# Kernel optimization log

Measured on AMD Instinct MI355X. Metric: run time of the kernel, lower is better.

Reference implementation:

```python
import jax, jax.numpy as jnp
import numpy as np

B, T, I, H, D, C, OUT = 32, 128, 64, 256, 32, 64, 32
DECAY = 0.99

def _lin(k, fi, fo):
    lim = 1.0 / np.sqrt(fi)
    kw, kb = jax.random.split(k)
    W = jax.random.uniform(kw, (fi, fo), minval=-lim, maxval=lim, dtype=jnp.float32)
    b = jax.random.uniform(kb, (fo,), minval=-lim, maxval=lim, dtype=jnp.float32)
    return W, b

def setup_inputs():
    key = jax.random.key(0)
    ks = jax.random.split(key, 12)
    x = jax.random.normal(ks[0], (B, T, I), dtype=jnp.float32)
    lengths = jax.random.randint(ks[1], (B,), 1, T + 1)
    W_dg1, b_dg1 = _lin(ks[2], I + H, D)
    W_dg2, b_dg2 = _lin(ks[3], D, D)
    W_e1, b_e1 = _lin(ks[4], 2 * I, H)
    W_e2, b_e2 = _lin(ks[5], H, H)
    W_ih, b_ih = _lin(ks[6], H, 3 * H)
    W_hh, b_hh = _lin(ks[7], H, 3 * H)
    W_f1, b_f1 = _lin(ks[8], H, H)
    W_f2, b_f2 = _lin(ks[9], H, C)
    return dict(x=x, lengths=lengths, out_lengths=OUT,
                W_dg1=W_dg1, b_dg1=b_dg1, W_dg2=W_dg2, b_dg2=b_dg2,
                W_e1=W_e1, b_e1=b_e1, W_e2=W_e2, b_e2=b_e2,
                W_ih=W_ih, b_ih=b_ih, W_hh=W_hh, b_hh=b_hh,
                W_f1=W_f1, b_f1=b_f1, W_f2=W_f2, b_f2=b_f2)

def _forward(x, lengths, out_lengths, W_dg1, b_dg1, W_dg2, b_dg2, W_e1, b_e1, W_e2, b_e2,
             W_ih, b_ih, W_hh, b_hh, W_f1, b_f1, W_f2, b_f2):
    Bs, Ts, Is = x.shape
    Ds = W_dg2.shape[1]
    Hs = W_e2.shape[1]
    decay = DECAY ** jnp.arange(1, Ds + 1, dtype=x.dtype)  # [D]
    d_idx = jnp.arange(Ds)
    gkey = jax.random.key(42)
    g_enc = jax.random.gumbel(jax.random.fold_in(gkey, 0), (Ts, Bs, Ds), x.dtype)
    g_dec = jax.random.gumbel(jax.random.fold_in(gkey, 1), (out_lengths, Bs, Ds), x.dtype)
    masks = (jnp.arange(Ts)[None, :] < lengths[:, None]).astype(x.dtype)  # [B,T]

    def gumbel_softmax_hard(logits, g):
        # F.gumbel_softmax(..., tau=1.0, hard=True) straight-through estimator
        y_soft = jax.nn.softmax(logits + g, axis=-1)
        y_hard = jax.nn.one_hot(jnp.argmax(y_soft, axis=-1), Ds, dtype=logits.dtype)
        return y_hard + y_soft - jax.lax.stop_gradient(y_soft)

    def gru_cell(xin, h):
        # torch.nn.GRUCell gate order: r, z, n
        gi = xin @ W_ih + b_ih
        gh = h @ W_hh + b_hh
        i_r, i_z, i_n = jnp.split(gi, 3, axis=-1)
        h_r, h_z, h_n = jnp.split(gh, 3, axis=-1)
        r = jax.nn.sigmoid(i_r + h_r)
        z = jax.nn.sigmoid(i_z + h_z)
        n = jnp.tanh(i_n + r * h_n)
        return (1.0 - z) * n + z * h

    def step_core(buf, h, x_t, g_t, mem_t):
        cell_in = jnp.concatenate([x_t, h], axis=-1)
        logits = jax.nn.elu(cell_in @ W_dg1 + b_dg1) @ W_dg2 + b_dg2
        gate = gumbel_softmax_hard(logits, g_t)  # [B,D]
        # shift buffer along dim 1 (new[:, :-1] = old[:, 1:], last slot zeroed)
        new_buf = jnp.concatenate([buf[:, 1:], jnp.zeros_like(buf[:, :1])], axis=1)
        upd = x_t[:, None, :] * decay[None, :, None] * gate[:, :, None]  # [B,D,I]
        new_buf = new_buf.at[:, d_idx, d_idx].set(upd)  # diagonal scatter-assign
        rnn_in = jnp.concatenate([x_t, mem_t], axis=-1)
        rnn_in = jax.nn.elu(rnn_in @ W_e1 + b_e1) @ W_e2 + b_e2
        return new_buf, gru_cell(rnn_in, h)

    buf0 = jnp.zeros((Bs, Ds + 1, Ds, Is), x.dtype)
    h0 = jnp.zeros((Bs, Hs), x.dtype)

    def enc_step(carry, inp):
        buf, h = carry
        x_t, m_t, g_t = inp
        mem_t = buf[:, 0].sum(axis=1)  # [B,I]
        buf, nh = step_core(buf, h, x_t, g_t, mem_t)
        h = m_t[:, None] * nh + (1.0 - m_t[:, None]) * h
        return (buf, h), None

    (buf, h), _ = jax.lax.scan(enc_step, (buf0, h0),
                               (jnp.swapaxes(x, 0, 1), masks.T, g_enc))

    x_zero = jnp.zeros((Bs, Is), x.dtype)

    def dec_step(carry, g_t):
        buf, h = carry
        # get_current_memory(slide=True): roll -1 along dim1 with last slot zeroed
        buf = jnp.concatenate([buf[:, 1:], jnp.zeros_like(buf[:, :1])], axis=1)
        mem_t = buf[:, 0].sum(axis=1)
        buf, nh = step_core(buf, h, x_zero, g_t, mem_t)
        out = jax.nn.relu(nh @ W_f1 + b_f1) @ W_f2 + b_f2
        return (buf, nh), out

    _, outs = jax.lax.scan(dec_step, (buf, h), g_dec)  # [OUT,B,C]
    return jnp.swapaxes(outs, 0, 1)  # [B,OUT,C]

def reference(x, lengths, out_lengths, W_dg1, b_dg1, W_dg2, b_dg2, W_e1, b_e1, W_e2, b_e2,
              W_ih, b_ih, W_hh, b_hh, W_f1, b_f1, W_f2, b_f2):
    return _forward(x, lengths, out_lengths, W_dg1, b_dg1, W_dg2, b_dg2, W_e1, b_e1,
                    W_e2, b_e2, W_ih, b_ih, W_hh, b_hh, W_f1, b_f1, W_f2, b_f2)
```

## Files before the change

### kernel.cpp

```cpp
#include <hip/hip_runtime.h>
#include <math.h>


#define kB 32
#define kT 128
#define kI 64
#define kH 256
#define kD 32
#define kC 64
#define kOut 32
#define kSteps (kT + kOut)
#define NB 89
#define NTHR 256
#define NT_ALL (NB * NTHR)

#define WS_FL    384
#define WS_H     1856
#define WS_SEL   (WS_H + 4*8192)
#define WS_MEM   (WS_SEL + 128)
#define WS_NZ    (WS_MEM + kB*kSteps*kI)
#define WS_LIN   WS_NZ
#define WS_O1    (WS_LIN + 4*8192)
#define WS_W2    (WS_O1 + 4*8192)
#define WS_B2    (WS_W2 + kH*3*kH)
#define WS_G     (WS_B2 + 3*kH)
#define WS_P     (WS_G + kT*kB*kD)
#define WS_ZERO_BYTES ((size_t)WS_NZ * sizeof(float))

__device__ __forceinline__ float cload(const float* p) {
  return __hip_atomic_load(p, __ATOMIC_RELAXED, __HIP_MEMORY_SCOPE_AGENT);
}
__device__ __forceinline__ void cstore(float* p, float v) {
  __hip_atomic_store(p, v, __ATOMIC_RELAXED, __HIP_MEMORY_SCOPE_AGENT);
}
__device__ __forceinline__ int cload_i(const int* p) {
  return __hip_atomic_load(p, __ATOMIC_RELAXED, __HIP_MEMORY_SCOPE_AGENT);
}
__device__ __forceinline__ void cstore_i(int* p, int v) {
  __hip_atomic_store(p, v, __ATOMIC_RELAXED, __HIP_MEMORY_SCOPE_AGENT);
}
__device__ __forceinline__ float4 cload4(const float* p) {
  float4 r;
  asm volatile("global_load_dwordx4 %0, %1, off sc0 sc1" : "=v"(r) : "v"(p));
  return r;
}
__device__ __forceinline__ void waitvm() {
  asm volatile("s_waitcnt vmcnt(0)" ::: "memory");
}

__device__ __forceinline__ void poll(const int* FL, int tid,
                                     int tH, int tDG, int tE, int tF1, int tF2) {
  int thr;
  if      (tid < 32) thr = tH;
  else if (tid == 32) thr = tDG;
  else if (tid < 65) thr = tE;
  else if (tid < 81) thr = tF1;
  else if (tid < 89) thr = tF2;
  else thr = 0;
  const int* p = FL + tid * 16;
  for (;;) {
    int ok = (thr <= 0) || (cload_i(p) >= thr);
    if (__syncthreads_count(ok) == NTHR) return;
    __builtin_amdgcn_s_sleep(2);
  }
}
__device__ __forceinline__ void setflag(int* FL, int tid, int idx, int val) {
  waitvm();
  __syncthreads();
  if (tid == 0) cstore_i(FL + idx * 16, val);
}

__device__ __forceinline__ void tf2x32(unsigned k0, unsigned k1,
                                       unsigned x0, unsigned x1,
                                       unsigned& o0, unsigned& o1) {
  unsigned ks2 = k0 ^ k1 ^ 0x1BD11BDAu;
  unsigned v0 = x0 + k0, v1 = x1 + k1;
#define TFR(r) { v0 += v1; v1 = (v1 << (r)) | (v1 >> (32-(r))); v1 ^= v0; }
  TFR(13) TFR(15) TFR(26) TFR(6)   v0 += k1;  v1 += ks2 + 1u;
  TFR(17) TFR(29) TFR(16) TFR(24)  v0 += ks2; v1 += k0  + 2u;
  TFR(13) TFR(15) TFR(26) TFR(6)   v0 += k0;  v1 += k1  + 3u;
  TFR(17) TFR(29) TFR(16) TFR(24)  v0 += k1;  v1 += ks2 + 4u;
  TFR(13) TFR(15) TFR(26) TFR(6)   v0 += ks2; v1 += k0  + 5u;
#undef TFR
  o0 = v0; o1 = v1;
}
__device__ __forceinline__ float bits_to_gumbel(unsigned bits) {
  float f = __uint_as_float((bits >> 9) | 0x3F800000u) - 1.0f;
  float u = f + 1.17549435e-38f;
  return -logf(-logf(u));
}

__device__ __forceinline__ void gridbar_full(unsigned* u, unsigned target) {
  __syncthreads();
  if (threadIdx.x == 0) {
    __threadfence();
    __hip_atomic_fetch_add(&u[320], 1u, __ATOMIC_ACQ_REL, __HIP_MEMORY_SCOPE_AGENT);
    while (__hip_atomic_load(&u[320], __ATOMIC_RELAXED, __HIP_MEMORY_SCOPE_AGENT) < target)
      __builtin_amdgcn_s_sleep(1);
    __threadfence();
  }
  __syncthreads();
}

__device__ __forceinline__ float elu1(float v) { return v > 0.f ? v : expm1f(v); }

__global__ __launch_bounds__(NTHR)
void delay_rnn(const float* __restrict__ x, const int* __restrict__ lengths,
               const float* __restrict__ W_dg1, const float* __restrict__ b_dg1,
               const float* __restrict__ W_dg2, const float* __restrict__ b_dg2,
               const float* __restrict__ W_e1,  const float* __restrict__ b_e1,
               const float* __restrict__ W_e2,  const float* __restrict__ b_e2,
               const float* __restrict__ W_ih,  const float* __restrict__ b_ih,
               const float* __restrict__ W_hh,  const float* __restrict__ b_hh,
               const float* __restrict__ W_f1,  const float* __restrict__ b_f1,
               const float* __restrict__ W_f2,  const float* __restrict__ b_f2,
               float* __restrict__ out, float* __restrict__ ws) {
  const int tid = threadIdx.x;
  const int bid = blockIdx.x;
  const int gid = bid * NTHR + tid;

  unsigned* baru = (unsigned*)ws;
  int*   FL    = (int*)(ws + WS_FL);
  float* hBuf  = ws + WS_H;
  int*   selG  = (int*)(ws + WS_SEL);
  float* mem   = ws + WS_MEM;
  float* linB  = ws + WS_LIN;
  float* o1B   = ws + WS_O1;
  float* W2g   = ws + WS_W2;
  float* B2g   = ws + WS_B2;
  float* g     = ws + WS_G;
  float* Pg    = ws + WS_P;

  __shared__ float S[35264];
  __shared__ float lgarr[1056];
  __shared__ float sb1[32], sb2[32], dec_sh[32];
  __shared__ int   sel[32], len_s[32];

  {
    unsigned k0, k1;
    tf2x32(0u, 42u, 0u, 0u, k0, k1);
    for (int i = gid; i < kT * kB * kD; i += NT_ALL) {
      unsigned a, b;
      tf2x32(k0, k1, 0u, (unsigned)i, a, b);
      g[i] = bits_to_gumbel(a ^ b);
    }
  }
  for (int idx = gid; idx < kH * 3 * kH; idx += NT_ALL) {
    int k = idx / (3 * kH), n = idx % (3 * kH);
    const float* wr = W_e2 + k * kH;
    float s0 = 0, s1 = 0, s2 = 0, s3 = 0;
    for (int m = 0; m < kH; m += 4) {
      float4 wv = *(const float4*)(wr + m);
      s0 += wv.x * W_ih[(m    ) * 3 * kH + n];
      s1 += wv.y * W_ih[(m + 1) * 3 * kH + n];
      s2 += wv.z * W_ih[(m + 2) * 3 * kH + n];
      s3 += wv.w * W_ih[(m + 3) * 3 * kH + n];
    }
    W2g[idx] = ((s0 + s1) + (s2 + s3));
  }
  for (int n = gid; n < 3 * kH; n += NT_ALL) {
    float s = b_ih[n];
    for (int m = 0; m < kH; ++m) s += b_e2[m] * W_ih[m * 3 * kH + n];
    B2g[n] = s;
  }
  for (int idx = gid; idx < kT * kB * kH; idx += NT_ALL) {
    int s = idx >> 13, r = idx & 8191, b = r >> 8, j = r & 255;
    const float* xr = x + (b * kT + s) * kI;
    float a0 = 0, a1 = 0, a2 = 0, a3 = 0;
    for (int k = 0; k < 64; k += 4) {
      float4 xv = *(const float4*)(xr + k);
      a0 += xv.x * W_e1[(64 + k) * 256 + j];
      a1 += xv.y * W_e1[(65 + k) * 256 + j];
      a2 += xv.z * W_e1[(66 + k) * 256 + j];
      a3 += xv.w * W_e1[(67 + k) * 256 + j];
    }
    Pg[idx] = ((a0 + a1) + (a2 + a3));
  }

  gridbar_full(baru, NB);

  if (bid < 32) {
    float* whh = S; float* w2 = S + 6240;
    const int jb = bid * 8;
    for (int i = tid; i < 6144; i += NTHR) {
      int gg = i >> 11, r = i & 2047, jj = r >> 8, k = r & 255;
      whh[(gg * 8 + jj) * 260 + k] = W_hh[k * 768 + gg * 256 + jb + jj];
      w2 [(gg * 8 + jj) * 260 + k] = W2g [k * 768 + gg * 256 + jb + jj];
    }
    if (tid < 24) { int gg = tid / 8, jj = tid % 8;
      sb1[tid] = b_hh[gg * 256 + jb + jj];
      sb2[tid] = B2g [gg * 256 + jb + jj];
    }
    if (tid < 32) len_s[tid] = lengths[tid];
    __syncthreads();

    float* sH = S + 12480; float* sLin = S + 20800;
    float* red = S + 29120;
    for (int s = 0; s < kSteps; ++s) {
      int tDG = (s >= 1) ? (s < kT ? s : kT) : 0;
      int tF1 = (s >= kT + 4) ? (s - 2) : 0;
      poll(FL, tid, s, tDG, s + 1, tF1, 0);

      const float* hR = hBuf + (s & 3) * 8192;
      const float* lR = linB + (s & 3) * 8192;
      const bool useC = (s >= 1 && s < kT);
      const float4* P4 = (const float4*)(Pg + (s - 1) * 8192);
      const int* selR = selG + ((s - 1) & 3) * 32;
      float4 th[8], tl[8], tp[8];
      int tsel[8];
      #pragma unroll
      for (int u8 = 0; u8 < 8; ++u8) {
        int i4 = (tid + u8 * 256) * 4;
        th[u8] = cload4(hR + i4);
        tl[u8] = cload4(lR + i4);
      }
      if (useC) {
        #pragma unroll
        for (int u8 = 0; u8 < 8; ++u8) {
          int idx = tid + u8 * 256; int b = idx >> 6, k4 = idx & 63;
          tp[u8] = P4[b * 64 + k4];
          tsel[u8] = cload_i(&selR[b]);
        }
      }
      waitvm();
      #pragma unroll
      for (int u8 = 0; u8 < 8; ++u8) {
        int idx = tid + u8 * 256; int b = idx >> 6, k4 = idx & 63;
        *(float4*)&sH[b * 260 + k4 * 4] = th[u8];
        float cx = 0.f, cy = 0.f, cz = 0.f, cw = 0.f;
        if (useC && tsel[u8] == 0) {
          cx = 0.99f * tp[u8].x; cy = 0.99f * tp[u8].y;
          cz = 0.99f * tp[u8].z; cw = 0.99f * tp[u8].w;
        }
        float4 v;
        v.x = elu1(tl[u8].x + cx);
        v.y = elu1(tl[u8].y + cy);
        v.z = elu1(tl[u8].z + cz);
        v.w = elu1(tl[u8].w + cw);
        *(float4*)&sLin[b * 260 + k4 * 4] = v;
      }
      __syncthreads();
      const float4* sH4 = (const float4*)sH;
      const float4* sL4 = (const float4*)sLin;
      const float4* wh4 = (const float4*)whh;
      const float4* w24 = (const float4*)w2;
      const int c  = tid & 7;
      const int b4 = (tid >> 3) & 7;
      const int kq = tid >> 6;
      float acc[24];
      #pragma unroll
      for (int a = 0; a < 24; ++a) acc[a] = 0.f;
      for (int kk = 0; kk < 16; ++kk) {
        int k4 = kq * 16 + kk;
        float4 wr[6];
        #pragma unroll
        for (int gg = 0; gg < 3; ++gg) {
          wr[gg]     = wh4[(gg * 8 + c) * 65 + k4];
          wr[3 + gg] = w24[(gg * 8 + c) * 65 + k4];
        }
        #pragma unroll
        for (int bi = 0; bi < 4; ++bi) {
          int b = bi * 8 + b4;
          float4 h4 = sH4[b * 65 + k4];
          float4 l4 = sL4[b * 65 + k4];
          #pragma unroll
          for (int gg = 0; gg < 3; ++gg) {
            float4 w = wr[gg];
            acc[bi * 6 + gg]     += h4.x * w.x + h4.y * w.y + h4.z * w.z + h4.w * w.w;
            w = wr[3 + gg];
            acc[bi * 6 + 3 + gg] += l4.x * w.x + l4.y * w.y + l4.z * w.z + l4.w * w.w;
          }
        }
      }
      #pragma unroll
      for (int bi = 0; bi < 4; ++bi)
        #pragma unroll
        for (int rr = 0; rr < 6; ++rr)
          red[kq * 1536 + rr * 256 + (bi * 8 + b4) * 8 + c] = acc[bi * 6 + rr];
      __syncthreads();
      {
        int b = tid >> 3, cc = tid & 7, jg = bid * 8 + cc;
        int lo = b * 8 + cc;
        float dots[6];
        #pragma unroll
        for (int rr = 0; rr < 6; ++rr)
          dots[rr] = (red[rr * 256 + lo] + red[1536 + rr * 256 + lo]) +
                     (red[3072 + rr * 256 + lo] + red[4608 + rr * 256 + lo]);
        float ghr = dots[0] + sb1[cc];
        float ghz = dots[1] + sb1[8 + cc];
        float ghn = dots[2] + sb1[16 + cc];
        float gir = dots[3] + sb2[cc];
        float giz = dots[4] + sb2[8 + cc];
        float gin = dots[5] + sb2[16 + cc];
        float r = 1.f / (1.f + expf(-(gir + ghr)));
        float z = 1.f / (1.f + expf(-(giz + ghz)));
        float n = tanhf(gin + r * ghn);
        float hold = sH[b * 260 + jg];
        float nh = (1.f - z) * n + z * hold;
        float hv = (s < kT) ? ((s < len_s[b]) ? nh : hold) : nh;
        cstore(&hBuf[((s + 1) & 3) * 8192 + b * 256 + jg], hv);
      }
      setflag(FL, tid, bid, s + 1);
    }
  }
  else if (bid < 64) {
    float* we1 = S;
    const int jb = (bid - 32) * 8;
    for (int i = tid; i < 1024; i += NTHR) {
      int jj = i >> 7, k = i & 127;
      we1[jj * 132 + k] = W_e1[k * 256 + jb + jj];
    }
    if (tid < 8) sb1[tid] = b_e1[jb + tid];
    __syncthreads();

    float* sx = S + 1056; float* sm = S + 3232;
    for (int e = 0; e < kSteps; ++e) {
      int tDG = e - 1 < 0 ? 0 : (e - 1 > kT ? kT : e - 1);
      poll(FL, tid, e - 2, tDG, 0, 0, 0);

      const bool encx = (e < kT);
      float4 tm[2];
      #pragma unroll
      for (int u2 = 0; u2 < 2; ++u2) {
        int idx = tid + u2 * 256; int b = idx >> 4, k4 = idx & 15;
        tm[u2] = cload4(mem + (b * kSteps + e) * kI + k4 * 4);
      }
      waitvm();
      #pragma unroll
      for (int u2 = 0; u2 < 2; ++u2) {
        int idx = tid + u2 * 256; int b = idx >> 4, k4 = idx & 15;
        *(float4*)&sm[b * 68 + k4 * 4] = tm[u2];
        if (encx)
          *(float4*)&sx[b * 68 + k4 * 4] =
              *(const float4*)(x + (b * kT + e) * kI + k4 * 4);
      }
      __syncthreads();
      const int b = tid >> 3, jj = tid & 7;
      const float4* sx4 = (const float4*)sx;
      const float4* sm4 = (const float4*)sm;
      const float4* w4p = (const float4*)we1;
      float a0 = 0, a1 = 0, a2 = 0, a3 = 0;
      if (encx) {
        for (int k4 = 0; k4 < 16; ++k4) {
          float4 xv = sx4[b * 17 + k4], w = w4p[jj * 33 + k4];
          a0 += xv.x * w.x; a1 += xv.y * w.y; a2 += xv.z * w.z; a3 += xv.w * w.w;
        }
      }
      for (int k4 = 0; k4 < 16; ++k4) {
        float4 mv = sm4[b * 17 + k4], w = w4p[jj * 33 + 16 + k4];
        a0 += mv.x * w.x; a1 += mv.y * w.y; a2 += mv.z * w.z; a3 += mv.w * w.w;
      }
      cstore(&linB[(e & 3) * 8192 + b * 256 + jb + jj],
             ((a0 + a1) + (a2 + a3)) + sb1[jj]);
      __syncthreads();
      setflag(FL, tid, 33 + (bid - 32), e + 1);
    }
  }
  else if (bid < 80) {
    float* wf1 = S;
    const int jb = (bid - 64) * 16;
    for (int i = tid; i < 4096; i += NTHR) {
      int jj = i >> 8, k = i & 255;
      wf1[jj * 260 + k] = W_f1[k * 256 + jb + jj];
    }
    if (tid < 16) sb1[tid] = b_f1[jb + tid];
    __syncthreads();

    float* sHf = S + 4160; float* red = S + 12480;
    for (int s = kT + 1; s <= kSteps; ++s) {
      int tF2 = (s >= kT + 5) ? (s - 2) : 0;
      poll(FL, tid, s, 0, 0, 0, tF2);

      const float* hR = hBuf + (s & 3) * 8192;
      float4 th[8];
      #pragma unroll
      for (int u8 = 0; u8 < 8; ++u8) th[u8] = cload4(hR + (tid + u8 * 256) * 4);
      waitvm();
      #pragma unroll
      for (int u8 = 0; u8 < 8; ++u8) {
        int idx = tid + u8 * 256; int b = idx >> 6, k4 = idx & 63;
        *(float4*)&sHf[b * 260 + k4 * 4] = th[u8];
      }
      __syncthreads();
      const float4* sH4 = (const float4*)sHf;
      const float4* w4p = (const float4*)wf1;
      const int cq = tid & 3, b4 = (tid >> 2) & 7, kq = tid >> 5;
      float acc[16];
      #pragma unroll
      for (int a = 0; a < 16; ++a) acc[a] = 0.f;
      for (int kk = 0; kk < 8; ++kk) {
        int k4 = kq * 8 + kk;
        float4 wr[4];
        #pragma unroll
        for (int ci = 0; ci < 4; ++ci) wr[ci] = w4p[(cq * 4 + ci) * 65 + k4];
        #pragma unroll
        for (int bi = 0; bi < 4; ++bi) {
          float4 h4 = sH4[(bi * 8 + b4) * 65 + k4];
          #pragma unroll
          for (int ci = 0; ci < 4; ++ci) {
            float4 w = wr[ci];
            acc[bi * 4 + ci] += h4.x * w.x + h4.y * w.y + h4.z * w.z + h4.w * w.w;
          }
        }
      }
      #pragma unroll
      for (int bi = 0; bi < 4; ++bi)
        #pragma unroll
        for (int ci = 0; ci < 4; ++ci)
          red[kq * 512 + (bi * 4 + ci) * 32 + cq * 8 + b4] = acc[bi * 4 + ci];
      __syncthreads();
      #pragma unroll
      for (int u2 = 0; u2 < 2; ++u2) {
        int o = tid * 2 + u2; int b = o >> 4, col = o & 15;
        int gg = ((b >> 3) * 4 + (col & 3)) * 32 + (col >> 2) * 8 + (b & 7);
        float v = 0.f;
        #pragma unroll
        for (int kq2 = 0; kq2 < 8; ++kq2) v += red[kq2 * 512 + gg];
        v += sb1[col];
        cstore(&o1B[(s & 3) * 8192 + b * 256 + (bid - 64) * 16 + col],
               v > 0.f ? v : 0.f);
      }
      __syncthreads();
      setflag(FL, tid, 65 + (bid - 64), s + 1);
    }
  }
  else if (bid < 88) {
    float* wf2 = S;
    const int cb = (bid - 80) * 8;
    for (int i = tid; i < 2048; i += NTHR) {
      int cc = i >> 8, k = i & 255;
      wf2[cc * 260 + k] = W_f2[k * 64 + cb + cc];
    }
    if (tid < 8) sb2[tid] = b_f2[cb + tid];
    __syncthreads();

    float* sO = S + 2080; float* red = S + 10400;
    for (int s = kT + 2; s <= kSteps + 1; ++s) {
      poll(FL, tid, 0, 0, 0, s, 0);

      const float* oR = o1B + ((s - 1) & 3) * 8192;
      float4 to[8];
      #pragma unroll
      for (int u8 = 0; u8 < 8; ++u8) to[u8] = cload4(oR + (tid + u8 * 256) * 4);
      waitvm();
      #pragma unroll
      for (int u8 = 0; u8 < 8; ++u8) {
        int idx = tid + u8 * 256; int b = idx >> 6, k4 = idx & 63;
        *(float4*)&sO[b * 260 + k4 * 4] = to[u8];
      }
      __syncthreads();
      const float4* sO4 = (const float4*)sO;
      const float4* w4p = (const float4*)wf2;
      const int c = tid & 7, b4 = (tid >> 3) & 7, kq = tid >> 6;
      float acc[4] = {0.f, 0.f, 0.f, 0.f};
      for (int kk = 0; kk < 16; ++kk) {
        int k4 = kq * 16 + kk;
        float4 w = w4p[c * 65 + k4];
        #pragma unroll
        for (int bi = 0; bi < 4; ++bi) {
          float4 o4 = sO4[(bi * 8 + b4) * 65 + k4];
          acc[bi] += o4.x * w.x + o4.y * w.y + o4.z * w.z + o4.w * w.w;
        }
      }
      #pragma unroll
      for (int bi = 0; bi < 4; ++bi)
        red[kq * 256 + bi * 64 + b4 * 8 + c] = acc[bi];
      __syncthreads();
      { int b = tid >> 3, col = tid & 7;
        int gg = (b >> 3) * 64 + (b & 7) * 8 + col;
        float v = (red[gg] + red[256 + gg]) + (red[512 + gg] + red[768 + gg]);
        out[(b * kOut + (s - 2 - kT)) * kC + (bid - 80) * 8 + col] =
            v + sb2[col];
      }
      __syncthreads();
      setflag(FL, tid, 81 + (bid - 80), s + 1);
    }
  }
  else {
    float* wdg1 = S; float* wdg2 = S + 10368;
    for (int i = tid; i < 10240; i += NTHR) {
      int j = i / 320, k = i % 320;
      wdg1[j * 324 + k] = W_dg1[k * 32 + j];
    }
    for (int i = tid; i < 1024; i += NTHR) wdg2[i] = W_dg2[i];
    if (tid < 32) { sb1[tid] = b_dg1[tid]; sb2[tid] = b_dg2[tid];
                    dec_sh[tid] = powf(0.99f, (float)(tid + 1)); }
    __syncthreads();

    float* sXH = S + 11392;
    float* red = S + 21760;
    float* l1s = S + 25856;
    for (int s = 0; s < kT; ++s) {
      poll(FL, tid, s, 0, 0, 0, 0);

      const float* hR = hBuf + (s & 3) * 8192;
      float4 th[8];
      #pragma unroll
      for (int u8 = 0; u8 < 8; ++u8) th[u8] = cload4(hR + (tid + u8 * 256) * 4);
      waitvm();
      #pragma unroll
      for (int u8 = 0; u8 < 8; ++u8) {
        int idx = tid + u8 * 256; int b = idx >> 6, k4 = idx & 63;
        *(float4*)&sXH[b * 324 + 64 + k4 * 4] = th[u8];
      }
      #pragma unroll
      for (int u2 = 0; u2 < 2; ++u2) {
        int idx = tid + u2 * 256; int b = idx >> 4, k4 = idx & 15;
        *(float4*)&sXH[b * 324 + k4 * 4] =
            *(const float4*)(x + (b * kT + s) * kI + k4 * 4);
      }
      __syncthreads();
      {
        const float4* sA4 = (const float4*)sXH;
        const float4* wd4 = (const float4*)wdg1;
        const int cq = tid & 7, b4 = (tid >> 3) & 7, kq = tid >> 6;
        float acc[16];
        #pragma unroll
        for (int a = 0; a < 16; ++a) acc[a] = 0.f;
        for (int kk = 0; kk < 20; ++kk) {
          int k4 = kq * 20 + kk;
          float4 wr[4];
          #pragma unroll
          for (int ci = 0; ci < 4; ++ci) wr[ci] = wd4[(cq * 4 + ci) * 81 + k4];
          #pragma unroll
          for (int bi = 0; bi < 4; ++bi) {
            float4 a4 = sA4[(bi * 8 + b4) * 81 + k4];
            #pragma unroll
            for (int ci = 0; ci < 4; ++ci) {
              float4 w = wr[ci];
              acc[bi * 4 + ci] += a4.x * w.x + a4.y * w.y + a4.z * w.z + a4.w * w.w;
            }
          }
        }
        #pragma unroll
        for (int bi = 0; bi < 4; ++bi)
          #pragma unroll
          for (int ci = 0; ci < 4; ++ci)
            red[kq * 1024 + (ci * 4 + bi) * 64 + cq * 8 + b4] = acc[bi * 4 + ci];
        __syncthreads();
        #pragma unroll
        for (int u4 = 0; u4 < 4; ++u4) {
          int o = tid * 4 + u4; int b = o >> 5, col = o & 31;
          int ci = col & 3, cq2 = col >> 2, bi = b >> 3, b42 = b & 7;
          int f = (ci * 4 + bi) * 64 + cq2 * 8 + b42;
          float v = (red[f] + red[1024 + f]) + (red[2048 + f] + red[3072 + f]);
          l1s[b * 36 + col] = elu1(v + sb1[col]);
        }
      }
      __syncthreads();
      for (int it = 0; it < 4; ++it) {
        int i = tid + it * 256; int b = i >> 5, j = i & 31;
        float sv = sb2[j];
        for (int k = 0; k < 32; ++k) sv += l1s[b * 36 + k] * wdg2[k * 32 + j];
        lgarr[b * 33 + j] = sv + g[(s * 32 + b) * 32 + j];
      }
      __syncthreads();
      if (tid < 32) {
        float best = lgarr[tid * 33]; int bi = 0;
        for (int j = 1; j < 32; ++j) {
          float v = lgarr[tid * 33 + j];
          if (v > best) { best = v; bi = j; }
        }
        sel[tid] = bi;
      }
      __syncthreads();
      if (tid < 32) cstore_i(&selG[(s & 3) * 32 + tid], sel[tid]);
      for (int it = 0; it < 8; ++it) {
        int i = tid + it * 256; int b = i >> 6, ii = i & 63;
        int d = sel[b];
        if (d > 0) {
          int c = s + 1 + d, e = -1;
          if (c < kT) e = c;
          else { int rr = c - kT - 1;
                 if (rr >= 0 && !(rr & 1)) { int kk = rr >> 1; if (kk < kOut) e = kT + kk; } }
          if (e >= 0) {
            float* p = &mem[(b * kSteps + e) * kI + ii];
            cstore(p, cload(p) + sXH[b * 324 + ii] * dec_sh[d]);
          }
        }
      }
      setflag(FL, tid, 32, s + 1);
    }
  }
}

extern "C" void kernel_launch(void* const* d_in, const int* in_sizes, int n_in,
                              void* d_out, int out_size, void* d_ws, size_t ws_size,
                              hipStream_t stream) {
  (void)in_sizes; (void)n_in; (void)out_size; (void)ws_size;
  const float* x      = (const float*)d_in[0];
  const int*   lens   = (const int*)  d_in[1];
  const float* W_dg1  = (const float*)d_in[3];
  const float* b_dg1  = (const float*)d_in[4];
  const float* W_dg2  = (const float*)d_in[5];
  const float* b_dg2  = (const float*)d_in[6];
  const float* W_e1   = (const float*)d_in[7];
  const float* b_e1   = (const float*)d_in[8];
  const float* W_e2   = (const float*)d_in[9];
  const float* b_e2   = (const float*)d_in[10];
  const float* W_ih   = (const float*)d_in[11];
  const float* b_ih   = (const float*)d_in[12];
  const float* W_hh   = (const float*)d_in[13];
  const float* b_hh   = (const float*)d_in[14];
  const float* W_f1   = (const float*)d_in[15];
  const float* b_f1   = (const float*)d_in[16];
  const float* W_f2   = (const float*)d_in[17];
  const float* b_f2   = (const float*)d_in[18];

  hipMemsetAsync(d_ws, 0, WS_ZERO_BYTES, stream);
  delay_rnn<<<dim3(NB), dim3(NTHR), 0, stream>>>(
      x, lens, W_dg1, b_dg1, W_dg2, b_dg2, W_e1, b_e1, W_e2, b_e2,
      W_ih, b_ih, W_hh, b_hh, W_f1, b_f1, W_f2, b_f2,
      (float*)d_out, (float*)d_ws);
}
```

Before: 1.941 ms.

## Precompute encoder layer-1 outputs and scatter memory contributions via linearity

Removes the 32 per-step encoder-linear blocks by precomputing x@W_e1+b_e1 for all steps up front. Because the memory input enters W_e1 linearly, the delay-gate block now adds decay times the precomputed memory projection (Pg) straight into the future step's precomputed linear output, instead of accumulating raw memory and recomputing the matmul each step. The grid shrinks from 89 to 57 blocks and the flag and poll layout is renumbered, so the GRU blocks no longer wait on an extra pipeline stage. In exchange, the delay-gate block does heavier read-modify-write traffic on global memory every step, and the up-front precompute grows.

```diff
diff --git a/kernel.cpp b/kernel.cpp
--- a/kernel.cpp
+++ b/kernel.cpp
@@ -10,21 +10,20 @@
 #define kC 64
 #define kOut 32
 #define kSteps (kT + kOut)
-#define NB 89
+#define NB 57
 #define NTHR 256
 #define NT_ALL (NB * NTHR)
 
 #define WS_FL    384
 #define WS_H     1856
 #define WS_SEL   (WS_H + 4*8192)
-#define WS_MEM   (WS_SEL + 128)
-#define WS_NZ    (WS_MEM + kB*kSteps*kI)
-#define WS_LIN   WS_NZ
-#define WS_O1    (WS_LIN + 4*8192)
-#define WS_W2    (WS_O1 + 4*8192)
+#define WS_NZ    (WS_SEL + 128)
+#define WS_W2    WS_NZ
 #define WS_B2    (WS_W2 + kH*3*kH)
 #define WS_G     (WS_B2 + 3*kH)
 #define WS_P     (WS_G + kT*kB*kD)
+#define WS_LINF  (WS_P + kT*kB*kH)
+#define WS_O1    (WS_LINF + kSteps*kB*kH)
 #define WS_ZERO_BYTES ((size_t)WS_NZ * sizeof(float))
 
 __device__ __forceinline__ float cload(const float* p) {
@@ -44,18 +43,22 @@
   asm volatile("global_load_dwordx4 %0, %1, off sc0 sc1" : "=v"(r) : "v"(p));
   return r;
 }
+__device__ __forceinline__ void cstore4(float* p, float4 v) {
+  cstore(p + 0, v.x); cstore(p + 1, v.y);
+  cstore(p + 2, v.z); cstore(p + 3, v.w);
+}
 __device__ __forceinline__ void waitvm() {
   asm volatile("s_waitcnt vmcnt(0)" ::: "memory");
 }
 
 __device__ __forceinline__ void poll(const int* FL, int tid,
-                                     int tH, int tDG, int tE, int tF1, int tF2) {
+                                     int tH, int tD, int tS, int tF1, int tF2) {
   int thr;
   if      (tid < 32) thr = tH;
-  else if (tid == 32) thr = tDG;
-  else if (tid < 65) thr = tE;
-  else if (tid < 81) thr = tF1;
-  else if (tid < 89) thr = tF2;
+  else if (tid == 32) thr = tD;
+  else if (tid == 33) thr = tS;
+  else if (tid < 50) thr = tF1;
+  else if (tid < 58) thr = tF2;
   else thr = 0;
   const int* p = FL + tid * 16;
   for (;;) {
@@ -123,18 +126,17 @@
   int*   FL    = (int*)(ws + WS_FL);
   float* hBuf  = ws + WS_H;
   int*   selG  = (int*)(ws + WS_SEL);
-  float* mem   = ws + WS_MEM;
-  float* linB  = ws + WS_LIN;
-  float* o1B   = ws + WS_O1;
   float* W2g   = ws + WS_W2;
   float* B2g   = ws + WS_B2;
   float* g     = ws + WS_G;
   float* Pg    = ws + WS_P;
+  float* linF  = ws + WS_LINF;
+  float* o1B   = ws + WS_O1;
 
   __shared__ float S[35264];
   __shared__ float lgarr[1056];
   __shared__ float sb1[32], sb2[32], dec_sh[32];
-  __shared__ int   sel[32], len_s[32];
+  __shared__ int   sel[32], len_s[32], edest[32];
 
   {
     unsigned k0, k1;
@@ -176,6 +178,23 @@
     }
     Pg[idx] = ((a0 + a1) + (a2 + a3));
   }
+  for (int idx = gid; idx < kSteps * kB * kH; idx += NT_ALL) {
+    int e = idx >> 13, r = idx & 8191, b = r >> 8, j = r & 255;
+    float v = b_e1[j];
+    if (e < kT) {
+      const float* xr = x + (b * kT + e) * kI;
+      float a0 = 0, a1 = 0, a2 = 0, a3 = 0;
+      for (int k = 0; k < 64; k += 4) {
+        float4 xv = *(const float4*)(xr + k);
+        a0 += xv.x * W_e1[(k    ) * 256 + j];
+        a1 += xv.y * W_e1[(k + 1) * 256 + j];
+        a2 += xv.z * W_e1[(k + 2) * 256 + j];
+        a3 += xv.w * W_e1[(k + 3) * 256 + j];
+      }
+      v += ((a0 + a1) + (a2 + a3));
+    }
+    linF[idx] = v;
+  }
 
   gridbar_full(baru, NB);
 
@@ -197,12 +216,13 @@
     float* sH = S + 12480; float* sLin = S + 20800;
     float* red = S + 29120;
     for (int s = 0; s < kSteps; ++s) {
-      int tDG = (s >= 1) ? (s < kT ? s : kT) : 0;
-      int tF1 = (s >= kT + 4) ? (s - 2) : 0;
-      poll(FL, tid, s, tDG, s + 1, tF1, 0);
+      int thrD = (s >= 2) ? ((s < kT) ? (s - 1) : kT) : 0;
+      int thrS = (s >= 1) ? ((s < kT) ? s : kT) : 0;
+      int tF1  = (s >= kT + 4) ? (s - 2) : 0;
+      poll(FL, tid, s, thrD, thrS, tF1, 0);
 
       const float* hR = hBuf + (s & 3) * 8192;
-      const float* lR = linB + (s & 3) * 8192;
+      const float* lR = linF + s * 8192;
       const bool useC = (s >= 1 && s < kT);
       const float4* P4 = (const float4*)(Pg + (s - 1) * 8192);
       const int* selR = selG + ((s - 1) & 3) * 32;
@@ -303,180 +323,7 @@
       setflag(FL, tid, bid, s + 1);
     }
   }
-  else if (bid < 64) {
-    float* we1 = S;
-    const int jb = (bid - 32) * 8;
-    for (int i = tid; i < 1024; i += NTHR) {
-      int jj = i >> 7, k = i & 127;
-      we1[jj * 132 + k] = W_e1[k * 256 + jb + jj];
-    }
-    if (tid < 8) sb1[tid] = b_e1[jb + tid];
-    __syncthreads();
-
-    float* sx = S + 1056; float* sm = S + 3232;
-    for (int e = 0; e < kSteps; ++e) {
-      int tDG = e - 1 < 0 ? 0 : (e - 1 > kT ? kT : e - 1);
-      poll(FL, tid, e - 2, tDG, 0, 0, 0);
-
-      const bool encx = (e < kT);
-      float4 tm[2];
-      #pragma unroll
-      for (int u2 = 0; u2 < 2; ++u2) {
-        int idx = tid + u2 * 256; int b = idx >> 4, k4 = idx & 15;
-        tm[u2] = cload4(mem + (b * kSteps + e) * kI + k4 * 4);
-      }
-      waitvm();
-      #pragma unroll
-      for (int u2 = 0; u2 < 2; ++u2) {
-        int idx = tid + u2 * 256; int b = idx >> 4, k4 = idx & 15;
-        *(float4*)&sm[b * 68 + k4 * 4] = tm[u2];
-        if (encx)
-          *(float4*)&sx[b * 68 + k4 * 4] =
-              *(const float4*)(x + (b * kT + e) * kI + k4 * 4);
-      }
-      __syncthreads();
-      const int b = tid >> 3, jj = tid & 7;
-      const float4* sx4 = (const float4*)sx;
-      const float4* sm4 = (const float4*)sm;
-      const float4* w4p = (const float4*)we1;
-      float a0 = 0, a1 = 0, a2 = 0, a3 = 0;
-      if (encx) {
-        for (int k4 = 0; k4 < 16; ++k4) {
-          float4 xv = sx4[b * 17 + k4], w = w4p[jj * 33 + k4];
-          a0 += xv.x * w.x; a1 += xv.y * w.y; a2 += xv.z * w.z; a3 += xv.w * w.w;
-        }
-      }
-      for (int k4 = 0; k4 < 16; ++k4) {
-        float4 mv = sm4[b * 17 + k4], w = w4p[jj * 33 + 16 + k4];
-        a0 += mv.x * w.x; a1 += mv.y * w.y; a2 += mv.z * w.z; a3 += mv.w * w.w;
-      }
-      cstore(&linB[(e & 3) * 8192 + b * 256 + jb + jj],
-             ((a0 + a1) + (a2 + a3)) + sb1[jj]);
-      __syncthreads();
-      setflag(FL, tid, 33 + (bid - 32), e + 1);
-    }
-  }
-  else if (bid < 80) {
-    float* wf1 = S;
-    const int jb = (bid - 64) * 16;
-    for (int i = tid; i < 4096; i += NTHR) {
-      int jj = i >> 8, k = i & 255;
-      wf1[jj * 260 + k] = W_f1[k * 256 + jb + jj];
-    }
-    if (tid < 16) sb1[tid] = b_f1[jb + tid];
-    __syncthreads();
-
-    float* sHf = S + 4160; float* red = S + 12480;
-    for (int s = kT + 1; s <= kSteps; ++s) {
-      int tF2 = (s >= kT + 5) ? (s - 2) : 0;
-      poll(FL, tid, s, 0, 0, 0, tF2);
-
-      const float* hR = hBuf + (s & 3) * 8192;
-      float4 th[8];
-      #pragma unroll
-      for (int u8 = 0; u8 < 8; ++u8) th[u8] = cload4(hR + (tid + u8 * 256) * 4);
-      waitvm();
-      #pragma unroll
-      for (int u8 = 0; u8 < 8; ++u8) {
-        int idx = tid + u8 * 256; int b = idx >> 6, k4 = idx & 63;
-        *(float4*)&sHf[b * 260 + k4 * 4] = th[u8];
-      }
-      __syncthreads();
-      const float4* sH4 = (const float4*)sHf;
-      const float4* w4p = (const float4*)wf1;
-      const int cq = tid & 3, b4 = (tid >> 2) & 7, kq = tid >> 5;
-      float acc[16];
-      #pragma unroll
-      for (int a = 0; a < 16; ++a) acc[a] = 0.f;
-      for (int kk = 0; kk < 8; ++kk) {
-        int k4 = kq * 8 + kk;
-        float4 wr[4];
-        #pragma unroll
-        for (int ci = 0; ci < 4; ++ci) wr[ci] = w4p[(cq * 4 + ci) * 65 + k4];
-        #pragma unroll
-        for (int bi = 0; bi < 4; ++bi) {
-          float4 h4 = sH4[(bi * 8 + b4) * 65 + k4];
-          #pragma unroll
-          for (int ci = 0; ci < 4; ++ci) {
-            float4 w = wr[ci];
-            acc[bi * 4 + ci] += h4.x * w.x + h4.y * w.y + h4.z * w.z + h4.w * w.w;
-          }
-        }
-      }
-      #pragma unroll
-      for (int bi = 0; bi < 4; ++bi)
-        #pragma unroll
-        for (int ci = 0; ci < 4; ++ci)
-          red[kq * 512 + (bi * 4 + ci) * 32 + cq * 8 + b4] = acc[bi * 4 + ci];
-      __syncthreads();
-      #pragma unroll
-      for (int u2 = 0; u2 < 2; ++u2) {
-        int o = tid * 2 + u2; int b = o >> 4, col = o & 15;
-        int gg = ((b >> 3) * 4 + (col & 3)) * 32 + (col >> 2) * 8 + (b & 7);
-        float v = 0.f;
-        #pragma unroll
-        for (int kq2 = 0; kq2 < 8; ++kq2) v += red[kq2 * 512 + gg];
-        v += sb1[col];
-        cstore(&o1B[(s & 3) * 8192 + b * 256 + (bid - 64) * 16 + col],
-               v > 0.f ? v : 0.f);
-      }
-      __syncthreads();
-      setflag(FL, tid, 65 + (bid - 64), s + 1);
-    }
-  }
-  else if (bid < 88) {
-    float* wf2 = S;
-    const int cb = (bid - 80) * 8;
-    for (int i = tid; i < 2048; i += NTHR) {
-      int cc = i >> 8, k = i & 255;
-      wf2[cc * 260 + k] = W_f2[k * 64 + cb + cc];
-    }
-    if (tid < 8) sb2[tid] = b_f2[cb + tid];
-    __syncthreads();
-
-    float* sO = S + 2080; float* red = S + 10400;
-    for (int s = kT + 2; s <= kSteps + 1; ++s) {
-      poll(FL, tid, 0, 0, 0, s, 0);
-
-      const float* oR = o1B + ((s - 1) & 3) * 8192;
-      float4 to[8];
-      #pragma unroll
-      for (int u8 = 0; u8 < 8; ++u8) to[u8] = cload4(oR + (tid + u8 * 256) * 4);
-      waitvm();
-      #pragma unroll
-      for (int u8 = 0; u8 < 8; ++u8) {
-        int idx = tid + u8 * 256; int b = idx >> 6, k4 = idx & 63;
-        *(float4*)&sO[b * 260 + k4 * 4] = to[u8];
-      }
-      __syncthreads();
-      const float4* sO4 = (const float4*)sO;
-      const float4* w4p = (const float4*)wf2;
-      const int c = tid & 7, b4 = (tid >> 3) & 7, kq = tid >> 6;
-      float acc[4] = {0.f, 0.f, 0.f, 0.f};
-      for (int kk = 0; kk < 16; ++kk) {
-        int k4 = kq * 16 + kk;
-        float4 w = w4p[c * 65 + k4];
-        #pragma unroll
-        for (int bi = 0; bi < 4; ++bi) {
-          float4 o4 = sO4[(bi * 8 + b4) * 65 + k4];
-          acc[bi] += o4.x * w.x + o4.y * w.y + o4.z * w.z + o4.w * w.w;
-        }
-      }
-      #pragma unroll
-      for (int bi = 0; bi < 4; ++bi)
-        red[kq * 256 + bi * 64 + b4 * 8 + c] = acc[bi];
-      __syncthreads();
-      { int b = tid >> 3, col = tid & 7;
-        int gg = (b >> 3) * 64 + (b & 7) * 8 + col;
-        float v = (red[gg] + red[256 + gg]) + (red[512 + gg] + red[768 + gg]);
-        out[(b * kOut + (s - 2 - kT)) * kC + (bid - 80) * 8 + col] =
-            v + sb2[col];
-      }
-      __syncthreads();
-      setflag(FL, tid, 81 + (bid - 80), s + 1);
-    }
-  }
-  else {
+  else if (bid == 32) {
     float* wdg1 = S; float* wdg2 = S + 10368;
     for (int i = tid; i < 10240; i += NTHR) {
       int j = i / 320, k = i % 320;
@@ -565,21 +412,166 @@
       }
       __syncthreads();
       if (tid < 32) cstore_i(&selG[(s & 3) * 32 + tid], sel[tid]);
-      for (int it = 0; it < 8; ++it) {
-        int i = tid + it * 256; int b = i >> 6, ii = i & 63;
-        int d = sel[b];
+      setflag(FL, tid, 33, s + 1);
+
+      if (tid < 32) {
+        int d = sel[tid], e = -1;
         if (d > 0) {
-          int c = s + 1 + d, e = -1;
+          int c = s + 1 + d;
           if (c < kT) e = c;
           else { int rr = c - kT - 1;
-                 if (rr >= 0 && !(rr & 1)) { int kk = rr >> 1; if (kk < kOut) e = kT + kk; } }
-          if (e >= 0) {
-            float* p = &mem[(b * kSteps + e) * kI + ii];
-            cstore(p, cload(p) + sXH[b * 324 + ii] * dec_sh[d]);
+                 if (rr >= 0 && !(rr & 1)) {
+                   int kk2 = rr >> 1; if (kk2 < kOut) e = kT + kk2; } }
+        }
+        edest[tid] = e;
+      }
+      __syncthreads();
+      {
+        float4 tv[8], tp2[8];
+        int te[8], tb2[8];
+        #pragma unroll
+        for (int it = 0; it < 8; ++it) {
+          int i = tid + it * 256; int b = i >> 6, q = i & 63;
+          te[it] = edest[b]; tb2[it] = b;
+          if (te[it] >= 0) {
+            tv[it]  = cload4(linF + te[it] * 8192 + b * 256 + q * 4);
+            tp2[it] = *(const float4*)(Pg + s * 8192 + b * 256 + q * 4);
           }
         }
+        waitvm();
+        #pragma unroll
+        for (int it = 0; it < 8; ++it) {
+          int i = tid + it * 256; int q = i & 63;
+          if (te[it] >= 0) {
+            float dec = dec_sh[sel[tb2[it]]];
+            float4 v = tv[it], p = tp2[it];
+            v.x += dec * p.x; v.y += dec * p.y;
+            v.z += dec * p.z; v.w += dec * p.w;
+            cstore4(linF + te[it] * 8192 + tb2[it] * 256 + q * 4, v);
+          }
+        }
       }
       setflag(FL, tid, 32, s + 1);
+    }
+  }
+  else if (bid < 49) {
+    float* wf1 = S;
+    const int jb = (bid - 33) * 16;
+    for (int i = tid; i < 4096; i += NTHR) {
+      int jj = i >> 8, k = i & 255;
+      wf1[jj * 260 + k] = W_f1[k * 256 + jb + jj];
+    }
+    if (tid < 16) sb1[tid] = b_f1[jb + tid];
+    __syncthreads();
+
+    float* sHf = S + 4160; float* red = S + 12480;
+    for (int s = kT + 1; s <= kSteps; ++s) {
+      int tF2 = (s >= kT + 5) ? (s - 2) : 0;
+      poll(FL, tid, s, 0, 0, 0, tF2);
+
+      const float* hR = hBuf + (s & 3) * 8192;
+      float4 th[8];
+      #pragma unroll
+      for (int u8 = 0; u8 < 8; ++u8) th[u8] = cload4(hR + (tid + u8 * 256) * 4);
+      waitvm();
+      #pragma unroll
+      for (int u8 = 0; u8 < 8; ++u8) {
+        int idx = tid + u8 * 256; int b = idx >> 6, k4 = idx & 63;
+        *(float4*)&sHf[b * 260 + k4 * 4] = th[u8];
+      }
+      __syncthreads();
+      const float4* sH4 = (const float4*)sHf;
+      const float4* w4p = (const float4*)wf1;
+      const int cq = tid & 3, b4 = (tid >> 2) & 7, kq = tid >> 5;
+      float acc[16];
+      #pragma unroll
+      for (int a = 0; a < 16; ++a) acc[a] = 0.f;
+      for (int kk = 0; kk < 8; ++kk) {
+        int k4 = kq * 8 + kk;
+        float4 wr[4];
+        #pragma unroll
+        for (int ci = 0; ci < 4; ++ci) wr[ci] = w4p[(cq * 4 + ci) * 65 + k4];
+        #pragma unroll
+        for (int bi = 0; bi < 4; ++bi) {
+          float4 h4 = sH4[(bi * 8 + b4) * 65 + k4];
+          #pragma unroll
+          for (int ci = 0; ci < 4; ++ci) {
+            float4 w = wr[ci];
+            acc[bi * 4 + ci] += h4.x * w.x + h4.y * w.y + h4.z * w.z + h4.w * w.w;
+          }
+        }
+      }
+      #pragma unroll
+      for (int bi = 0; bi < 4; ++bi)
+        #pragma unroll
+        for (int ci = 0; ci < 4; ++ci)
+          red[kq * 512 + (bi * 4 + ci) * 32 + cq * 8 + b4] = acc[bi * 4 + ci];
+      __syncthreads();
+      #pragma unroll
+      for (int u2 = 0; u2 < 2; ++u2) {
+        int o = tid * 2 + u2; int b = o >> 4, col = o & 15;
+        int gg = ((b >> 3) * 4 + (col & 3)) * 32 + (col >> 2) * 8 + (b & 7);
+        float v = 0.f;
+        #pragma unroll
+        for (int kq2 = 0; kq2 < 8; ++kq2) v += red[kq2 * 512 + gg];
+        v += sb1[col];
+        cstore(&o1B[(s & 3) * 8192 + b * 256 + (bid - 33) * 16 + col],
+               v > 0.f ? v : 0.f);
+      }
+      __syncthreads();
+      setflag(FL, tid, bid + 1, s + 1);
+    }
+  }
+  else {
+    float* wf2 = S;
+    const int cb = (bid - 49) * 8;
+    for (int i = tid; i < 2048; i += NTHR) {
+      int cc = i >> 8, k = i & 255;
+      wf2[cc * 260 + k] = W_f2[k * 64 + cb + cc];
+    }
+    if (tid < 8) sb2[tid] = b_f2[cb + tid];
+    __syncthreads();
+
+    float* sO = S + 2080; float* red = S + 10400;
+    for (int s = kT + 2; s <= kSteps + 1; ++s) {
+      poll(FL, tid, 0, 0, 0, s, 0);
+
+      const float* oR = o1B + ((s - 1) & 3) * 8192;
+      float4 to[8];
+      #pragma unroll
+      for (int u8 = 0; u8 < 8; ++u8) to[u8] = cload4(oR + (tid + u8 * 256) * 4);
+      waitvm();
+      #pragma unroll
+      for (int u8 = 0; u8 < 8; ++u8) {
+        int idx = tid + u8 * 256; int b = idx >> 6, k4 = idx & 63;
+        *(float4*)&sO[b * 260 + k4 * 4] = to[u8];
+      }
+      __syncthreads();
+      const float4* sO4 = (const float4*)sO;
+      const float4* w4p = (const float4*)wf2;
+      const int c = tid & 7, b4 = (tid >> 3) & 7, kq = tid >> 6;
+      float acc[4] = {0.f, 0.f, 0.f, 0.f};
+      for (int kk = 0; kk < 16; ++kk) {
+        int k4 = kq * 16 + kk;
+        float4 w = w4p[c * 65 + k4];
+        #pragma unroll
+        for (int bi = 0; bi < 4; ++bi) {
+          float4 o4 = sO4[(bi * 8 + b4) * 65 + k4];
+          acc[bi] += o4.x * w.x + o4.y * w.y + o4.z * w.z + o4.w * w.w;
+        }
+      }
+      #pragma unroll
+      for (int bi = 0; bi < 4; ++bi)
+        red[kq * 256 + bi * 64 + b4 * 8 + c] = acc[bi];
+      __syncthreads();
+      { int b = tid >> 3, col = tid & 7;
+        int gg = (b >> 3) * 64 + (b & 7) * 8 + col;
+        float v = (red[gg] + red[256 + gg]) + (red[512 + gg] + red[768 + gg]);
+        out[(b * kOut + (s - 2 - kT)) * kC + (bid - 49) * 8 + col] =
+            v + sb2[col];
+      }
+      __syncthreads();
+      setflag(FL, tid, bid + 1, s + 1);
     }
   }
 }
```

After: 2.251 ms. 15.9% more time.
